# Performance work log

Hardware: AMD Instinct MI355X
Metric: run time of the kernel (lower is better)

Reference implementation:

```python
import jax, jax.numpy as jnp
import numpy as np

B, H, K, D = 4096, 3, 32768, 128


def setup_inputs() -> dict:
    key = jax.random.key(0)
    k_in, k_emb = jax.random.split(key)
    inputs = jax.random.normal(k_in, (B, 1, D), dtype=jnp.float32)
    # xavier-uniform-ish init with per-head decay 0.5**h (gain 6.0), as in the module
    ks = jax.random.split(k_emb, H)
    tables = []
    for h in range(H):
        gain = 6.0 * (0.5 ** h)
        bound = gain * np.sqrt(6.0 / (K + D))
        tables.append(jax.random.uniform(ks[h], (K, D), jnp.float32, -bound, bound))
    emb = jnp.stack(tables, axis=0)  # [H, K, D]
    return {"inputs": inputs, "emb": emb}


def reference(inputs, emb):
    # Eval-mode HRQ forward: per-head negative squared-L2 distances to the
    # codebook on the running residual, hard argmax assignment, summed codes.
    x = inputs[:, 0, :]                      # [B, D]
    n_heads = emb.shape[0]
    resid = x
    quantized = jnp.zeros_like(x)
    codes = []
    for h in range(n_heads):
        W = emb[h]                            # [K, D]
        # -(||r||^2 + ||w||^2 - 2 r.w)  -> argmax == nearest code
        dists = -(jnp.sum(resid * resid, axis=1, keepdims=True)
                  + jnp.sum(W * W, axis=1)
                  - 2.0 * resid @ W.T)        # [B, K]
        c = jnp.argmax(dists, axis=-1)        # [B]
        q = jnp.take(W, c, axis=0)            # onehot(c) @ W == gather
        resid = resid - q
        quantized = quantized + q
        codes.append(c)
    loss = jnp.zeros(x.shape[0], dtype=inputs.dtype)
    return loss, quantized.reshape(inputs.shape), jnp.stack(codes, axis=1)
```

## Files before the change

### kernel.cpp

```cpp
#include <hip/hip_runtime.h>
#include <math.h>

#define NB 4096
#define NH 3
#define NK 32768
#define ND 128
#define KE 384
#define RB 64
#define CS 8
#define CPB (NK / CS)
#define CI 256
#define NCI (CPB / CI)

typedef _Float16 half8_t __attribute__((ext_vector_type(8)));
typedef float f32x4 __attribute__((ext_vector_type(4)));
typedef __attribute__((address_space(1))) const unsigned int gu32_t;
typedef __attribute__((address_space(3))) unsigned int lu32_t;

__global__ __launch_bounds__(64) void init_kernel(const float* __restrict__ inp,
                                                  float* __restrict__ resid,
                                                  float* __restrict__ rr,
                                                  float* __restrict__ out) {
  int row = blockIdx.x;
  int lane = threadIdx.x;
  const float2* ip = (const float2*)(inp + row * ND);
  float2 v = ip[lane];
  ((float2*)(resid + row * ND))[lane] = v;
  ((float2*)(out + NB + row * ND))[lane] = make_float2(0.f, 0.f);
  if (lane == 0) out[row] = 0.f;
  float s = v.x * v.x + v.y * v.y;
  #pragma unroll
  for (int m = 32; m; m >>= 1) s += __shfl_xor(s, m, 64);
  if (lane == 0) rr[row] = s;
}

__global__ __launch_bounds__(256) void norms_kernel(const float* __restrict__ emb,
                                                    float* __restrict__ norms) {
  int row = blockIdx.x * 4 + (threadIdx.x >> 6);
  int lane = threadIdx.x & 63;
  const float2* wp = (const float2*)(emb + (size_t)row * ND);
  float2 v = wp[lane];
  float s = v.x * v.x + v.y * v.y;
  #pragma unroll
  for (int m = 32; m; m >>= 1) s += __shfl_xor(s, m, 64);
  if (lane == 0) norms[row] = s;
}

__global__ __launch_bounds__(256) void split_w_kernel(const float* __restrict__ W,
                                                      _Float16* __restrict__ Bext) {
  const int cg = blockIdx.x;
  const int n_lo = threadIdx.x & 15;
  const int c = threadIdx.x >> 4;
  const int n = cg * 16 + n_lo;

  const float4* wp = (const float4*)(W + (size_t)n * ND + c * 8);
  float4 v0 = wp[0], v1 = wp[1];
  float xv[8] = {v0.x, v0.y, v0.z, v0.w, v1.x, v1.y, v1.z, v1.w};
  half8_t h, l;
  #pragma unroll
  for (int j = 0; j < 8; ++j) {
    _Float16 hh = (_Float16)xv[j];
    h[j] = hh;
    l[j] = (_Float16)(xv[j] - (float)hh);
  }
  _Float16* base = Bext + ((size_t)cg * 12 + (c >> 2)) * 512 + (c & 3) * 128 + n_lo * 8;
  *(half8_t*)(base) = h;
  *(half8_t*)(base + 2048) = l;
  *(half8_t*)(base + 4096) = h;
}

__global__ __launch_bounds__(256) void split_a_kernel(const float* __restrict__ resid,
                                                      _Float16* __restrict__ Aext) {
  int idx = blockIdx.x * 256 + threadIdx.x;
  int r = idx >> 7, k = idx & 127;
  float x = resid[idx];
  _Float16 h = (_Float16)x;
  _Float16 l = (_Float16)(x - (float)h);
  size_t base = (size_t)r * KE;
  Aext[base + k] = h;
  Aext[base + 128 + k] = h;
  Aext[base + 256 + k] = l;
}

__global__ __launch_bounds__(256, 2) void score_mfma_kernel(
    const _Float16* __restrict__ Aext, const _Float16* __restrict__ Bext,
    const float* __restrict__ rr, const float* __restrict__ normh,
    float* __restrict__ partial_s, int* __restrict__ partial_i) {
  __shared__ __align__(16) _Float16 Ash[RB * KE];

  const int bid = blockIdx.x;
  const int cs = bid & 7;
  const int rowb = bid >> 3;
  const int rowBase = rowb * RB;
  const int colBase0 = cs * CPB;

  const int tid = threadIdx.x;
  const int lane = tid & 63;
  const int wn = tid >> 6;
  const int l15 = lane & 15;
  const int q = lane >> 4;

  {
    const int mrow = lane >> 3;
    const int cg = (lane & 7) ^ (mrow & 7);
    #pragma unroll
    for (int i = 0; i < 12; ++i) {
      int wc = wn * 12 + i;
      int p = wc >> 3;
      int m0 = (wc & 7) * 8;
      const _Float16* gA = Aext + (size_t)(rowBase + m0 + mrow) * KE + p * 64 + cg * 8;
      __builtin_amdgcn_global_load_lds((gu32_t*)gA, (lu32_t*)&Ash[(p * 64 + m0) * 64], 16, 0, 0);
    }
  }

  int aaddr[2][4];
  #pragma unroll
  for (int par = 0; par < 2; ++par)
    #pragma unroll
    for (int mt = 0; mt < 4; ++mt) {
      int m = mt * 16 + l15;
      int slot = (par * 4 + q) ^ (m & 7);
      aaddr[par][mt] = (m * 8 + slot) * 16;
    }

  float rv[16];
  #pragma unroll
  for (int mt = 0; mt < 4; ++mt)
    #pragma unroll
    for (int reg = 0; reg < 4; ++reg)
      rv[mt * 4 + reg] = rr[rowBase + mt * 16 + q * 4 + reg];

  float bs[16];
  int bi[16];
  #pragma unroll
  for (int t = 0; t < 16; ++t) { bs[t] = -INFINITY; bi[t] = 0x7fffffff; }

  __syncthreads();

  #pragma unroll 1
  for (int ci = 0; ci < NCI; ++ci) {
    const int ncol = colBase0 + ci * CI + wn * 64;
    const _Float16* bcol = Bext + ((size_t)(ncol >> 4) * 12) * 512 + lane * 8;

    f32x4 acc[4][4];
    #pragma unroll
    for (int i = 0; i < 4; ++i)
      #pragma unroll
      for (int j = 0; j < 4; ++j) acc[i][j] = (f32x4){0.f, 0.f, 0.f, 0.f};

    #pragma unroll 4
    for (int ks = 0; ks < 12; ++ks) {
      half8_t bf[4];
      #pragma unroll
      for (int tn = 0; tn < 4; ++tn)
        bf[tn] = *(const half8_t*)(bcol + (tn * 12 + ks) * 512);
      half8_t af[4];
      #pragma unroll
      for (int mt = 0; mt < 4; ++mt)
        af[mt] = *(const half8_t*)((const char*)Ash + aaddr[ks & 1][mt] + (ks >> 1) * 8192);
      #pragma unroll
      for (int mt = 0; mt < 4; ++mt)
        #pragma unroll
        for (int tn = 0; tn < 4; ++tn)
          acc[mt][tn] = __builtin_amdgcn_mfma_f32_16x16x32_f16(af[mt], bf[tn], acc[mt][tn], 0, 0, 0);
    }

    #pragma unroll
    for (int tn = 0; tn < 4; ++tn) {
      float nw = normh[ncol + tn * 16 + l15];
      int cidx = ncol + tn * 16 + l15;
      #pragma unroll
      for (int mt = 0; mt < 4; ++mt) {
        #pragma unroll
        for (int reg = 0; reg < 4; ++reg) {
          const int s = mt * 4 + reg;
          float t1 = rv[s] + nw;
          float v = fmaf(2.0f, acc[mt][tn][reg], -t1);
          if (v > bs[s] || (v == bs[s] && cidx < bi[s])) { bs[s] = v; bi[s] = cidx; }
        }
      }
    }
  }

  __syncthreads();
  float* red_s = (float*)Ash;
  int* red_i = (int*)Ash + RB * 4;
  #pragma unroll
  for (int t = 0; t < 16; ++t) {
    float s = bs[t];
    int ii = bi[t];
    #pragma unroll
    for (int mask = 1; mask <= 8; mask <<= 1) {
      float os = __shfl_xor(s, mask, 64);
      int oi = __shfl_xor(ii, mask, 64);
      if (os > s || (os == s && oi < ii)) { s = os; ii = oi; }
    }
    if (l15 == 0) {
      int rloc = (t >> 2) * 16 + q * 4 + (t & 3);
      red_s[rloc * 4 + wn] = s;
      red_i[rloc * 4 + wn] = ii;
    }
  }
  __syncthreads();
  if (tid < RB) {
    float s0 = red_s[tid * 4];
    int i0 = red_i[tid * 4];
    #pragma unroll
    for (int x = 1; x < 4; ++x) {
      float sx = red_s[tid * 4 + x];
      int ix = red_i[tid * 4 + x];
      if (sx > s0 || (sx == s0 && ix < i0)) { s0 = sx; i0 = ix; }
    }
    partial_s[(size_t)(rowBase + tid) * CS + cs] = s0;
    partial_i[(size_t)(rowBase + tid) * CS + cs] = i0;
  }
}

__global__ __launch_bounds__(64) void reduce_update_kernel(const float* __restrict__ embh,
                                                           float* __restrict__ resid,
                                                           float* __restrict__ rr,
                                                           const float* __restrict__ ps,
                                                           const int* __restrict__ pi,
                                                           float* __restrict__ out, int h) {
  int row = blockIdx.x;
  int lane = threadIdx.x;
  float bs = -INFINITY;
  int bi = 0x7fffffff;
  if (lane < CS) {
    bs = ps[(size_t)row * CS + lane];
    bi = pi[(size_t)row * CS + lane];
  }
  #pragma unroll
  for (int m = 4; m; m >>= 1) {
    float os = __shfl_xor(bs, m, 64);
    int oi = __shfl_xor(bi, m, 64);
    if (os > bs || (os == bs && oi < bi)) { bs = os; bi = oi; }
  }
  int c = __shfl(bi, 0, 64);
  if (lane == 0) out[NB + NB * ND + row * NH + h] = (float)c;

  const float* wv = embh + (size_t)c * ND;
  float q0 = wv[lane], q1 = wv[lane + 64];
  float r0 = resid[row * ND + lane] - q0;
  float r1 = resid[row * ND + lane + 64] - q1;
  resid[row * ND + lane] = r0;
  resid[row * ND + lane + 64] = r1;
  out[NB + row * ND + lane] += q0;
  out[NB + row * ND + lane + 64] += q1;
  float s = r0 * r0 + r1 * r1;
  #pragma unroll
  for (int m = 32; m; m >>= 1) s += __shfl_xor(s, m, 64);
  if (lane == 0) rr[row] = s;
}

extern "C" void kernel_launch(void* const* d_in, const int* in_sizes, int n_in,
                              void* d_out, int out_size, void* d_ws, size_t ws_size,
                              hipStream_t stream) {
  const float* inp = (const float*)d_in[0];
  const float* emb = (const float*)d_in[1];
  float* out = (float*)d_out;

  float* resid = (float*)d_ws;
  float* rr = resid + NB * ND;
  float* norms = rr + NB;
  float* ps = norms + NH * NK;
  int* pi = (int*)(ps + (size_t)NB * CS);
  _Float16* Aext = (_Float16*)(pi + (size_t)NB * CS);
  _Float16* Bext = Aext + (size_t)NB * KE;

  hipLaunchKernelGGL(init_kernel, dim3(NB), dim3(64), 0, stream, inp, resid, rr, out);
  hipLaunchKernelGGL(norms_kernel, dim3(NH * NK / 4), dim3(256), 0, stream, emb, norms);
  for (int h = 0; h < NH; ++h) {
    hipLaunchKernelGGL(split_a_kernel, dim3(NB * ND / 256), dim3(256), 0, stream, resid, Aext);
    hipLaunchKernelGGL(split_w_kernel, dim3(NK / 16), dim3(256), 0, stream,
                       emb + (size_t)h * NK * ND, Bext);
    hipLaunchKernelGGL(score_mfma_kernel, dim3((NB / RB) * CS), dim3(256), 0, stream,
                       Aext, Bext, rr, norms + (size_t)h * NK, ps, pi);
    hipLaunchKernelGGL(reduce_update_kernel, dim3(NB), dim3(64), 0, stream,
                       emb + (size_t)h * NK * ND, resid, rr, ps, pi, out, h);
  }
}
```

Measured before the change: 471.0 us.

## Fuse A-split into init/update, double-buffer B fragments, raise column splits

Removes the separate split_a kernel by writing the fp16 hi/lo residual split directly in init_kernel and reduce_update_kernel, saving one launch and one pass over the residual per head. The score kernel now prefetches the next k-step's B fragments into registers while the current MFMAs run, and it walks column chunks in reverse so a `>=` comparison keeps the lowest index on ties with cheaper logic. Column splits rise from 8 to 16 and launch bounds from 2 to 3 blocks per SM, giving more blocks in flight. The cost is more register pressure and a larger partial-result reduction.

```diff
diff --git a/kernel.cpp b/kernel.cpp
--- a/kernel.cpp
+++ b/kernel.cpp
@@ -7,12 +7,13 @@
 #define ND 128
 #define KE 384
 #define RB 64
-#define CS 8
+#define CS 16
 #define CPB (NK / CS)
 #define CI 256
 #define NCI (CPB / CI)
 
 typedef _Float16 half8_t __attribute__((ext_vector_type(8)));
+typedef _Float16 half2_t __attribute__((ext_vector_type(2)));
 typedef float f32x4 __attribute__((ext_vector_type(4)));
 typedef __attribute__((address_space(1))) const unsigned int gu32_t;
 typedef __attribute__((address_space(3))) unsigned int lu32_t;
@@ -20,7 +21,8 @@
 __global__ __launch_bounds__(64) void init_kernel(const float* __restrict__ inp,
                                                   float* __restrict__ resid,
                                                   float* __restrict__ rr,
-                                                  float* __restrict__ out) {
+                                                  float* __restrict__ out,
+                                                  _Float16* __restrict__ Aext) {
   int row = blockIdx.x;
   int lane = threadIdx.x;
   const float2* ip = (const float2*)(inp + row * ND);
@@ -28,6 +30,13 @@
   ((float2*)(resid + row * ND))[lane] = v;
   ((float2*)(out + NB + row * ND))[lane] = make_float2(0.f, 0.f);
   if (lane == 0) out[row] = 0.f;
+  _Float16 h0 = (_Float16)v.x, h1 = (_Float16)v.y;
+  _Float16 l0 = (_Float16)(v.x - (float)h0), l1 = (_Float16)(v.y - (float)h1);
+  half2_t h = {h0, h1}, l = {l0, l1};
+  _Float16* base = Aext + (size_t)row * KE;
+  *(half2_t*)(base + 2 * lane) = h;
+  *(half2_t*)(base + 128 + 2 * lane) = h;
+  *(half2_t*)(base + 256 + 2 * lane) = l;
   float s = v.x * v.x + v.y * v.y;
   #pragma unroll
   for (int m = 32; m; m >>= 1) s += __shfl_xor(s, m, 64);
@@ -69,28 +78,15 @@
   *(half8_t*)(base + 4096) = h;
 }
 
-__global__ __launch_bounds__(256) void split_a_kernel(const float* __restrict__ resid,
-                                                      _Float16* __restrict__ Aext) {
-  int idx = blockIdx.x * 256 + threadIdx.x;
-  int r = idx >> 7, k = idx & 127;
-  float x = resid[idx];
-  _Float16 h = (_Float16)x;
-  _Float16 l = (_Float16)(x - (float)h);
-  size_t base = (size_t)r * KE;
-  Aext[base + k] = h;
-  Aext[base + 128 + k] = h;
-  Aext[base + 256 + k] = l;
-}
-
-__global__ __launch_bounds__(256, 2) void score_mfma_kernel(
+__global__ __launch_bounds__(256, 3) void score_mfma_kernel(
     const _Float16* __restrict__ Aext, const _Float16* __restrict__ Bext,
     const float* __restrict__ rr, const float* __restrict__ normh,
     float* __restrict__ partial_s, int* __restrict__ partial_i) {
   __shared__ __align__(16) _Float16 Ash[RB * KE];
 
   const int bid = blockIdx.x;
-  const int cs = bid & 7;
-  const int rowb = bid >> 3;
+  const int cs = bid & 15;
+  const int rowb = bid >> 4;
   const int rowBase = rowb * RB;
   const int colBase0 = cs * CPB;
 
@@ -137,8 +133,16 @@
 
   __syncthreads();
 
+  half8_t bfc[4];
+  {
+    const _Float16* b0 =
+        Bext + ((size_t)((colBase0 + (NCI - 1) * CI + wn * 64) >> 4) * 12) * 512 + lane * 8;
+    #pragma unroll
+    for (int tn = 0; tn < 4; ++tn) bfc[tn] = *(const half8_t*)(b0 + tn * 12 * 512);
+  }
+
   #pragma unroll 1
-  for (int ci = 0; ci < NCI; ++ci) {
+  for (int ci = NCI - 1; ci >= 0; --ci) {
     const int ncol = colBase0 + ci * CI + wn * 64;
     const _Float16* bcol = Bext + ((size_t)(ncol >> 4) * 12) * 512 + lane * 8;
 
@@ -148,25 +152,31 @@
       #pragma unroll
       for (int j = 0; j < 4; ++j) acc[i][j] = (f32x4){0.f, 0.f, 0.f, 0.f};
 
-    #pragma unroll 4
+    #pragma unroll 2
     for (int ks = 0; ks < 12; ++ks) {
-      half8_t bf[4];
-      #pragma unroll
-      for (int tn = 0; tn < 4; ++tn)
-        bf[tn] = *(const half8_t*)(bcol + (tn * 12 + ks) * 512);
+      const _Float16* bn = (ks < 11) ? (bcol + (ks + 1) * 512)
+                                     : (ci ? (bcol - (CI / 16) * 12 * 512) : bcol);
+      half8_t bfn[4];
+      #pragma unroll
+      for (int tn = 0; tn < 4; ++tn) bfn[tn] = *(const half8_t*)(bn + tn * 12 * 512);
+
       half8_t af[4];
       #pragma unroll
       for (int mt = 0; mt < 4; ++mt)
         af[mt] = *(const half8_t*)((const char*)Ash + aaddr[ks & 1][mt] + (ks >> 1) * 8192);
+
       #pragma unroll
       for (int mt = 0; mt < 4; ++mt)
         #pragma unroll
         for (int tn = 0; tn < 4; ++tn)
-          acc[mt][tn] = __builtin_amdgcn_mfma_f32_16x16x32_f16(af[mt], bf[tn], acc[mt][tn], 0, 0, 0);
-    }
-
-    #pragma unroll
-    for (int tn = 0; tn < 4; ++tn) {
+          acc[mt][tn] = __builtin_amdgcn_mfma_f32_16x16x32_f16(af[mt], bfc[tn], acc[mt][tn], 0, 0, 0);
+
+      #pragma unroll
+      for (int tn = 0; tn < 4; ++tn) bfc[tn] = bfn[tn];
+    }
+
+    #pragma unroll
+    for (int tn = 3; tn >= 0; --tn) {
       float nw = normh[ncol + tn * 16 + l15];
       int cidx = ncol + tn * 16 + l15;
       #pragma unroll
@@ -176,7 +186,7 @@
           const int s = mt * 4 + reg;
           float t1 = rv[s] + nw;
           float v = fmaf(2.0f, acc[mt][tn][reg], -t1);
-          if (v > bs[s] || (v == bs[s] && cidx < bi[s])) { bs[s] = v; bi[s] = cidx; }
+          if (v >= bs[s]) { bs[s] = v; bi[s] = cidx; }
         }
       }
     }
@@ -221,7 +231,8 @@
                                                            float* __restrict__ rr,
                                                            const float* __restrict__ ps,
                                                            const int* __restrict__ pi,
-                                                           float* __restrict__ out, int h) {
+                                                           float* __restrict__ out,
+                                                           _Float16* __restrict__ Aext, int h) {
   int row = blockIdx.x;
   int lane = threadIdx.x;
   float bs = -INFINITY;
@@ -231,7 +242,7 @@
     bi = pi[(size_t)row * CS + lane];
   }
   #pragma unroll
-  for (int m = 4; m; m >>= 1) {
+  for (int m = 8; m; m >>= 1) {
     float os = __shfl_xor(bs, m, 64);
     int oi = __shfl_xor(bi, m, 64);
     if (os > bs || (os == bs && oi < bi)) { bs = os; bi = oi; }
@@ -247,6 +258,14 @@
   resid[row * ND + lane + 64] = r1;
   out[NB + row * ND + lane] += q0;
   out[NB + row * ND + lane + 64] += q1;
+
+  _Float16 h0 = (_Float16)r0, l0 = (_Float16)(r0 - (float)h0);
+  _Float16 h1 = (_Float16)r1, l1 = (_Float16)(r1 - (float)h1);
+  _Float16* ab = Aext + (size_t)row * KE;
+  ab[lane] = h0;       ab[lane + 64] = h1;
+  ab[128 + lane] = h0; ab[128 + lane + 64] = h1;
+  ab[256 + lane] = l0; ab[256 + lane + 64] = l1;
+
   float s = r0 * r0 + r1 * r1;
   #pragma unroll
   for (int m = 32; m; m >>= 1) s += __shfl_xor(s, m, 64);
@@ -268,15 +287,14 @@
   _Float16* Aext = (_Float16*)(pi + (size_t)NB * CS);
   _Float16* Bext = Aext + (size_t)NB * KE;
 
-  hipLaunchKernelGGL(init_kernel, dim3(NB), dim3(64), 0, stream, inp, resid, rr, out);
+  hipLaunchKernelGGL(init_kernel, dim3(NB), dim3(64), 0, stream, inp, resid, rr, out, Aext);
   hipLaunchKernelGGL(norms_kernel, dim3(NH * NK / 4), dim3(256), 0, stream, emb, norms);
   for (int h = 0; h < NH; ++h) {
-    hipLaunchKernelGGL(split_a_kernel, dim3(NB * ND / 256), dim3(256), 0, stream, resid, Aext);
     hipLaunchKernelGGL(split_w_kernel, dim3(NK / 16), dim3(256), 0, stream,
                        emb + (size_t)h * NK * ND, Bext);
     hipLaunchKernelGGL(score_mfma_kernel, dim3((NB / RB) * CS), dim3(256), 0, stream,
                        Aext, Bext, rr, norms + (size_t)h * NK, ps, pi);
     hipLaunchKernelGGL(reduce_update_kernel, dim3(NB), dim3(64), 0, stream,
-                       emb + (size_t)h * NK * ND, resid, rr, ps, pi, out, h);
-  }
-}
+                       emb + (size_t)h * NK * ND, resid, rr, ps, pi, out, Aext, h);
+  }
+}
```

After: 535.5 us. 13.7% more time.
